# Kernel optimization log

Hardware: AMD Instinct MI355X
Metric: run time of the kernel (lower is better)

The kernel has to match this reference:

```python
import jax, jax.numpy as jnp
import numpy as np

B, N, D, H = 4, 4096, 512, 8
K = D // H  # per-head dim = 64


def setup_inputs() -> dict:
    key = jax.random.key(0)
    k1, k2, k3, k4 = jax.random.split(key, 4)
    x = jax.random.normal(k1, (B, N, D), dtype=jnp.float32)
    # Conv1d(D, K, 1, bias=False) -> weight matrix [K, D], kaiming fan_out
    Wa = jax.random.normal(k2, (K, D), dtype=jnp.float32) * np.float32(np.sqrt(2.0 / K))
    # Conv1d(K, 1, 1) -> weight vector [K], bias scalar (init 0.01)
    Wb = jax.random.normal(k3, (K,), dtype=jnp.float32) * np.float32(np.sqrt(2.0))
    Wc = jax.random.normal(k4, (K,), dtype=jnp.float32) * np.float32(np.sqrt(2.0))
    wb_bias = jnp.full((), 0.01, dtype=jnp.float32)
    wc_bias = jnp.full((), 0.01, dtype=jnp.float32)
    bias = jnp.full((K,), 0.01, dtype=jnp.float32)
    return {"batchinput": x, "Wa": Wa, "Wb": Wb, "wb_bias": wb_bias,
            "Wc": Wc, "wc_bias": wc_bias, "bias": bias}


def reference(batchinput, Wa, Wb, wb_bias, Wc, wc_bias, bias):
    # single step (n_steps=1); all n_head heads share weights, so mean over
    # identical heads equals one head (dropout=0.0 -> identity).
    h = jnp.einsum('bnd,kd->bnk', batchinput, Wa)            # [B,N,K] projected feats
    t1 = jnp.einsum('bnk,k->bn', h, Wb) + wb_bias            # [B,N]
    t2 = jnp.einsum('bnk,k->bn', h, Wc) + wc_bias            # [B,N]
    scores = t1[:, :, None] + t2[:, None, :]                 # [B,N,N] additive score
    coefs = jax.nn.softmax(jax.nn.leaky_relu(scores, negative_slope=0.2), axis=-1)
    out = jnp.einsum('bnm,bmk->bnk', coefs, h) + bias        # [B,N,K]
    return out
```

## Files before the change

kernel.cpp:

```cpp
#include <hip/hip_runtime.h>
#include <hip/hip_bf16.h>

constexpr int cB = 4;
constexpr int cN = 4096;
constexpr int cD = 512;
constexpr int cK = 64;
constexpr int cNB = cB * cN;
constexpr int cNP = cN + 1;
constexpr int cCS = 16;
constexpr int cNC = cN / cCS;
constexpr int cNC1 = cNC + 1;

typedef unsigned short u16;
typedef unsigned int u32;
typedef unsigned long long u64;
typedef __bf16 bf16x8 __attribute__((ext_vector_type(8)));
typedef float f32x4 __attribute__((ext_vector_type(4)));

constexpr size_t OFF_H    = 0;
constexpr size_t OFF_T1   = OFF_H    + (size_t)cNB * cK;
constexpr size_t OFF_T2   = OFF_T1   + cNB;
constexpr size_t OFF_T2S  = OFF_T2   + cNB;
constexpr size_t OFF_IDX  = OFF_T2S  + cNB;
constexpr size_t OFF_P    = OFF_IDX  + cNB;
constexpr size_t OFF_EPL  = OFF_P    + cNB;
constexpr size_t OFF_GNL  = OFF_EPL  + (size_t)cB * cNP * cK;
constexpr size_t OFF_EPS  = OFF_GNL  + (size_t)cB * cNP * cK;
constexpr size_t OFF_GNS  = OFF_EPS  + (size_t)cB * cNP;
constexpr size_t OFF_CHE  = OFF_GNS  + (size_t)cB * cNP;
constexpr size_t OFF_CHG  = OFF_CHE  + (size_t)cB * cNC * cK;
constexpr size_t OFF_CHES = OFF_CHG  + (size_t)cB * cNC * cK;
constexpr size_t OFF_CHGS = OFF_CHES + (size_t)cB * cNC;
constexpr size_t OFF_OFE  = OFF_CHGS + (size_t)cB * cNC;
constexpr size_t OFF_OFG  = OFF_OFE  + (size_t)cB * cNC1 * cK;
constexpr size_t OFF_OFES = OFF_OFG  + (size_t)cB * cNC1 * cK;
constexpr size_t OFF_OFGS = OFF_OFES + (size_t)cB * cNC1;
constexpr size_t OFF_WB16 = OFF_OFGS + (size_t)cB * cNC1;

__device__ __forceinline__ u16 f2bf(float f) {
    unsigned u = __float_as_uint(f);
    u += 0x7fffu + ((u >> 16) & 1u);
    return (u16)(u >> 16);
}
__device__ __forceinline__ u32 pk2(float a, float b) {
    return (u32)f2bf(a) | ((u32)f2bf(b) << 16);
}
__device__ __forceinline__ u32 f2sort(float f) {
    u32 b = __float_as_uint(f);
    u32 mask = (u32)((int)b >> 31);
    return b ^ (mask | 0x80000000u);
}

__global__ __launch_bounds__(256) void k_prep(
    const float* __restrict__ x, const float* __restrict__ Wa,
    const float* __restrict__ Wb, const float* __restrict__ wbb,
    const float* __restrict__ Wc, const float* __restrict__ wcb,
    u16* __restrict__ wab16, float* __restrict__ t1, float* __restrict__ t2)
{
    __shared__ float wabL[cD], wacL[cD];
    int t = threadIdx.x;
    if (blockIdx.x >= 512) {
        int i4 = (((int)blockIdx.x - 512) * 256 + t) * 4;
        float4 v = *(const float4*)(Wa + i4);
        uint2 p = {pk2(v.x, v.y), pk2(v.z, v.w)};
        *(uint2*)(wab16 + i4) = p;
        return;
    }
    float s1a = 0.f, s2a = 0.f, s1b = 0.f, s2b = 0.f;
#pragma unroll 8
    for (int k = 0; k < cK; ++k) {
        float wbk = Wb[k], wck = Wc[k];
        float wa1 = Wa[k * cD + t];
        float wa2 = Wa[k * cD + t + 256];
        s1a += wa1 * wbk; s2a += wa1 * wck;
        s1b += wa2 * wbk; s2b += wa2 * wck;
    }
    wabL[t] = s1a; wacL[t] = s2a; wabL[t + 256] = s1b; wacL[t + 256] = s2b;
    __syncthreads();

    int w = t >> 6, lane = t & 63;
    int d1 = lane * 4, d2 = 256 + lane * 4;
    float4 wbA = *(const float4*)&wabL[d1], wbB = *(const float4*)&wabL[d2];
    float4 wcA = *(const float4*)&wacL[d1], wcB = *(const float4*)&wacL[d2];
    float wbbv = wbb[0], wcbv = wcb[0];
#pragma unroll 2
    for (int rr = 0; rr < 8; ++rr) {
        int row = blockIdx.x * 32 + w * 8 + rr;
        const float* xp = x + (size_t)row * cD;
        float4 a  = *(const float4*)(xp + d1);
        float4 bq = *(const float4*)(xp + d2);
        float p1 = a.x*wbA.x + a.y*wbA.y + a.z*wbA.z + a.w*wbA.w
                 + bq.x*wbB.x + bq.y*wbB.y + bq.z*wbB.z + bq.w*wbB.w;
        float p2 = a.x*wcA.x + a.y*wcA.y + a.z*wcA.z + a.w*wcA.w
                 + bq.x*wcB.x + bq.y*wcB.y + bq.z*wcB.z + bq.w*wcB.w;
#pragma unroll
        for (int off = 32; off > 0; off >>= 1) {
            p1 += __shfl_down(p1, off, 64);
            p2 += __shfl_down(p2, off, 64);
        }
        if (lane == 0) { t1[row] = p1 + wbbv; t2[row] = p2 + wcbv; }
    }
}

__global__ __launch_bounds__(256) void k_projrank(
    const float* __restrict__ x, const u16* __restrict__ wab16,
    const float* __restrict__ t1, const float* __restrict__ t2,
    float* __restrict__ h, float* __restrict__ t2s, int* __restrict__ idxs,
    int* __restrict__ pidx)
{
    __shared__ __align__(16) u64 shbuf[4096 + 256];
    int t = threadIdx.x;
    if (blockIdx.x < 256) {
        int rowbase = blockIdx.x * 64;
        int w = t >> 6, lane = t & 63, m = lane & 15, quad = lane >> 4;
        const float* xg = x + (size_t)(rowbase + w * 16 + m) * cD + quad * 8;
        const u16* wg = wab16 + (size_t)m * cD + quad * 8;

        f32x4 acc[4] = {{0.f,0.f,0.f,0.f},{0.f,0.f,0.f,0.f},
                        {0.f,0.f,0.f,0.f},{0.f,0.f,0.f,0.f}};
#pragma unroll 4
        for (int s = 0; s < 16; ++s) {
            float4 xa  = *(const float4*)(xg + s * 32);
            float4 xb2 = *(const float4*)(xg + s * 32 + 4);
            uint4 xv = {pk2(xa.x, xa.y), pk2(xa.z, xa.w),
                        pk2(xb2.x, xb2.y), pk2(xb2.z, xb2.w)};
            bf16x8 av;
            __builtin_memcpy(&av, &xv, 16);
#pragma unroll
            for (int g = 0; g < 4; ++g) {
                uint4 wv = *(const uint4*)(wg + (size_t)g * 16 * cD + s * 32);
                bf16x8 bv;
                __builtin_memcpy(&bv, &wv, 16);
                acc[g] = __builtin_amdgcn_mfma_f32_16x16x32_bf16(av, bv, acc[g], 0, 0, 0);
            }
        }
#pragma unroll
        for (int g = 0; g < 4; ++g) {
#pragma unroll
            for (int r4 = 0; r4 < 4; ++r4) {
                int row = w * 16 + quad * 4 + r4;
                h[(size_t)(rowbase + row) * cK + g * 16 + m] = acc[g][r4];
            }
        }
    } else {
        u64* keys = shbuf;
        int* part = (int*)(shbuf + 4096);
        int rb = blockIdx.x - 256;
        int b = rb >> 6;
        int rowgrp = rb & 63;
        for (int i = t; i < cN; i += 256)
            keys[i] = ((u64)f2sort(t2[b * cN + i]) << 32) | (u32)i;
        __syncthreads();
        int lane = t & 63, subset = t >> 6;
        int myrow = rowgrp * 64 + lane;
        u64 mykey = keys[myrow];
        u32 pk_hi = f2sort(-t1[(size_t)b * cN + myrow]);
        int s0 = subset * 1024;
        int cnt = 0, cnt2 = 0;
#pragma unroll 8
        for (int kk = 0; kk < 1024; ++kk) {
            u64 kv = keys[s0 + kk];
            cnt  += (kv < mykey) ? 1 : 0;
            cnt2 += ((u32)(kv >> 32) < pk_hi) ? 1 : 0;
        }
        part[subset * 64 + lane] = cnt;
        part[256 + subset * 64 + lane] = cnt2;
        __syncthreads();
        if (t < 64) {
            int jj = rowgrp * 64 + t;
            int rank = part[t] + part[64 + t] + part[128 + t] + part[192 + t];
            int pc   = part[256 + t] + part[320 + t] + part[384 + t] + part[448 + t];
            t2s[b * cN + rank] = t2[b * cN + jj];
            idxs[b * cN + rank] = jj;
            pidx[b * cN + jj] = pc;
        }
    }
}

__global__ __launch_bounds__(128) void k_chunkscan(
    const float* __restrict__ t2s, const int* __restrict__ idxs,
    const float* __restrict__ h,
    float* __restrict__ EpL, float* __restrict__ GnL,
    float* __restrict__ eps_l, float* __restrict__ gns_l,
    float* __restrict__ chE, float* __restrict__ chG,
    float* __restrict__ chEs, float* __restrict__ chGs)
{
    __shared__ float hs[cCS][cK];
    int t = threadIdx.x;
    int lane = t & 63, w = t >> 6;
    int unit = blockIdx.x;
    int c = unit & (cNC - 1);
    int b = unit >> 8;
    int base = b * cN + c * cCS;
    size_t rowbase = ((size_t)b * cNP + c * cCS) * cK;
    int sbase = b * cNP + c * cCS;
    float M2 = t2s[b * cN + cN - 1];
    int   idxv = (lane < 8) ? idxs[base + w * 8 + lane] : 0;
    float t2v  = (lane < cCS) ? t2s[base + lane] : 0.f;

#pragma unroll
    for (int ii = 0; ii < 8; ++ii) {
        int j = __shfl(idxv, ii, 64);
        hs[w * 8 + ii][lane] = h[((size_t)b * cN + j) * cK + lane];
    }
    float slope = w ? 0.2f : 1.0f;
    float ev[cCS];
#pragma unroll
    for (int i = 0; i < cCS; ++i)
        ev[i] = __expf(slope * (__shfl(t2v, i, 64) - M2));
    __syncthreads();

    if (w == 0) {
        if (c == cNC - 1) {
            EpL[((size_t)b * cNP + cN) * cK + lane] = 0.f;
            if (lane == 0) eps_l[b * cNP + cN] = 0.f;
        }
        float acc = 0.f, accs = 0.f;
#pragma unroll
        for (int i = cCS - 1; i >= 0; --i) {
            acc += ev[i] * hs[i][lane]; accs += ev[i];
            EpL[rowbase + (size_t)i * cK + lane] = acc;
            if (lane == 0) eps_l[sbase + i] = accs;
        }
        chE[((size_t)b * cNC + c) * cK + lane] = acc;
        if (lane == 0) chEs[b * cNC + c] = accs;
    } else {
        if (c == cNC - 1) {
            GnL[((size_t)b * cNP + cN) * cK + lane] = 0.f;
            if (lane == 0) gns_l[b * cNP + cN] = 0.f;
        }
        float acc = 0.f, accs = 0.f;
#pragma unroll
        for (int i = 0; i < cCS; ++i) {
            GnL[rowbase + (size_t)i * cK + lane] = acc;
            if (lane == 0) gns_l[sbase + i] = accs;
            acc += ev[i] * hs[i][lane]; accs += ev[i];
        }
        chG[((size_t)b * cNC + c) * cK + lane] = acc;
        if (lane == 0) chGs[b * cNC + c] = accs;
    }
}

constexpr unsigned SMEM_OUT = 134664;
__global__ __launch_bounds__(256, 1) void k_outf(
    const float* __restrict__ t1, const float* __restrict__ t2s,
    const int* __restrict__ pidx,
    const float* __restrict__ EpL, const float* __restrict__ GnL,
    const float* __restrict__ eps_l, const float* __restrict__ gns_l,
    const float* __restrict__ chE, const float* __restrict__ chG,
    const float* __restrict__ chEs, const float* __restrict__ chGs,
    const float* __restrict__ bias, float* __restrict__ out)
{
    extern __shared__ char sm[];
    float (*ofEl)[64] = (float(*)[64])(sm);
    float (*ofGl)[64] = (float(*)[64])(sm + 65792);
    float* ofEsL      = (float*)(sm + 131584);
    float* ofGsL      = (float*)(sm + 132612);
    float (*wsum)[64] = (float(*)[64])(sm + 133640);

    int t = threadIdx.x, lane = t & 63, w = t >> 6;
    int blk = blockIdx.x;
    int b = blk >> 6;
    const float* chEb = chE + (size_t)b * cNC * cK;
    const float* chGb = chG + (size_t)b * cNC * cK;
    int c0 = w * 64;

    {
        float cv[64]; float s = 0.f;
#pragma unroll
        for (int i = 0; i < 64; ++i) { cv[i] = chEb[(size_t)(c0 + i) * cK + lane]; s += cv[i]; }
        wsum[w][lane] = s;
        if (w == 0) {
            float e0 = chEs[b*cNC + lane*4+0], e1 = chEs[b*cNC + lane*4+1];
            float e2 = chEs[b*cNC + lane*4+2], e3 = chEs[b*cNC + lane*4+3];
            float p = e0+e1+e2+e3, s2 = p;
#pragma unroll
            for (int off = 1; off < 64; off <<= 1) {
                float tv = __shfl_down(s2, off, 64);
                if (lane + off < 64) s2 += tv;
            }
            float excl = s2 - p;
            ofEsL[lane*4+0] = excl + e1 + e2 + e3;
            ofEsL[lane*4+1] = excl + e2 + e3;
            ofEsL[lane*4+2] = excl + e3;
            ofEsL[lane*4+3] = excl;
            if (lane == 0) ofEsL[cNC] = 0.f;
        } else if (w == 1) {
            float e0 = chGs[b*cNC + lane*4+0], e1 = chGs[b*cNC + lane*4+1];
            float e2 = chGs[b*cNC + lane*4+2], e3 = chGs[b*cNC + lane*4+3];
            float p = e0+e1+e2+e3, s2 = p;
#pragma unroll
            for (int off = 1; off < 64; off <<= 1) {
                float tv = __shfl_up(s2, off, 64);
                if (lane >= off) s2 += tv;
            }
            float excl = s2 - p;
            ofGsL[lane*4+0] = excl;
            ofGsL[lane*4+1] = excl + e0;
            ofGsL[lane*4+2] = excl + e0 + e1;
            ofGsL[lane*4+3] = excl + e0 + e1 + e2;
            if (lane == 63) ofGsL[cNC] = s2;
        }
        __syncthreads();
        float base = 0.f;
        for (int w2 = w + 1; w2 < 4; ++w2) base += wsum[w2][lane];
        float run = base;
#pragma unroll
        for (int i = 63; i >= 0; --i) { ofEl[c0 + i][lane] = run; run += cv[i]; }
        if (w == 0) ofEl[cNC][lane] = 0.f;
    }
    __syncthreads();
    {
        float cv[64]; float s = 0.f;
#pragma unroll
        for (int i = 0; i < 64; ++i) { cv[i] = chGb[(size_t)(c0 + i) * cK + lane]; s += cv[i]; }
        wsum[w][lane] = s;
        __syncthreads();
        float base = 0.f;
        for (int w2 = 0; w2 < w; ++w2) base += wsum[w2][lane];
        float run = base;
#pragma unroll
        for (int i = 0; i < 64; ++i) { ofGl[c0 + i][lane] = run; run += cv[i]; }
        if (w == 3) ofGl[cNC][lane] = run;
    }
    __syncthreads();

    float bv = bias[lane];
    float M2 = t2s[(size_t)b * cN + cN - 1];
    int r0 = blk * 64 + w * 16;
    const float* epsb = eps_l + (size_t)b * cNP;
    const float* gnsb = gns_l + (size_t)b * cNP;
#pragma unroll 8
    for (int i = 0; i < 16; ++i) {
        int r = r0 + i;
        float T1 = t1[r];
        float smax = T1 + M2;
        float m = fmaxf(smax, 0.2f * smax);
        float A  = __expf(smax - m);
        float Cc = __expf(0.2f * smax - m);
        int p = pidx[r];
        int c = p >> 4;
        size_t pr = ((size_t)b * cNP + p) * cK + lane;
        float num = A * (EpL[pr] + ofEl[c][lane]) + Cc * (GnL[pr] + ofGl[c][lane]);
        float den = A * (epsb[p] + ofEsL[c]) + Cc * (gnsb[p] + ofGsL[c]);
        out[(size_t)r * cK + lane] = num / den + bv;
    }
}

__global__ __launch_bounds__(1024) void k_offsets(
    const float* __restrict__ chE, const float* __restrict__ chG,
    const float* __restrict__ chEs, const float* __restrict__ chGs,
    float* __restrict__ ofE, float* __restrict__ ofG,
    float* __restrict__ ofEs, float* __restrict__ ofGs)
{
    __shared__ float wsum[16][64];
    int t = threadIdx.x;
    int lane = t & 63, w = t >> 6;
    int dir = blockIdx.x & 1;
    int b = blockIdx.x >> 1;
    const float* ch = dir ? chG : chE;
    float* of = dir ? ofG : ofE;
    int c0 = w * 16;

    float cv[16];
    float s = 0.f;
#pragma unroll
    for (int i = 0; i < 16; ++i) {
        cv[i] = ch[((size_t)b * cNC + c0 + i) * cK + lane];
        s += cv[i];
    }
    wsum[w][lane] = s;
    __syncthreads();
    float base = 0.f;
    if (dir == 0) { for (int w2 = w + 1; w2 < 16; ++w2) base += wsum[w2][lane]; }
    else          { for (int w2 = 0; w2 < w; ++w2) base += wsum[w2][lane]; }

    if (dir == 0) {
        float run = base;
#pragma unroll
        for (int i = 15; i >= 0; --i) {
            of[((size_t)b * cNC1 + c0 + i) * cK + lane] = run;
            run += cv[i];
        }
        if (w == 0) of[((size_t)b * cNC1 + cNC) * cK + lane] = 0.f;
    } else {
        float run = base;
#pragma unroll
        for (int i = 0; i < 16; ++i) {
            of[((size_t)b * cNC1 + c0 + i) * cK + lane] = run;
            run += cv[i];
        }
        if (w == 15) of[((size_t)b * cNC1 + cNC) * cK + lane] = run;
    }

    if (w == 0) {
        const float* chs = dir ? chGs : chEs;
        float* ofs = dir ? ofGs : ofEs;
        float e0 = chs[b * cNC + lane * 4 + 0];
        float e1 = chs[b * cNC + lane * 4 + 1];
        float e2 = chs[b * cNC + lane * 4 + 2];
        float e3 = chs[b * cNC + lane * 4 + 3];
        float p = e0 + e1 + e2 + e3;
        if (dir == 0) {
            float s2 = p;
#pragma unroll
            for (int off = 1; off < 64; off <<= 1) {
                float tv = __shfl_down(s2, off, 64);
                if (lane + off < 64) s2 += tv;
            }
            float excl = s2 - p;
            ofs[b * cNC1 + lane * 4 + 0] = excl + e1 + e2 + e3;
            ofs[b * cNC1 + lane * 4 + 1] = excl + e2 + e3;
            ofs[b * cNC1 + lane * 4 + 2] = excl + e3;
            ofs[b * cNC1 + lane * 4 + 3] = excl;
            if (lane == 0) ofs[b * cNC1 + cNC] = 0.f;
        } else {
            float s2 = p;
#pragma unroll
            for (int off = 1; off < 64; off <<= 1) {
                float tv = __shfl_up(s2, off, 64);
                if (lane >= off) s2 += tv;
            }
            float excl = s2 - p;
            ofs[b * cNC1 + lane * 4 + 0] = excl;
            ofs[b * cNC1 + lane * 4 + 1] = excl + e0;
            ofs[b * cNC1 + lane * 4 + 2] = excl + e0 + e1;
            ofs[b * cNC1 + lane * 4 + 3] = excl + e0 + e1 + e2;
            if (lane == 63) ofs[b * cNC1 + cNC] = s2;
        }
    }
}

__global__ __launch_bounds__(256) void k_out(
    const float* __restrict__ t1, const float* __restrict__ t2s,
    const int* __restrict__ pidx,
    const float* __restrict__ EpL, const float* __restrict__ GnL,
    const float* __restrict__ eps_l, const float* __restrict__ gns_l,
    const float* __restrict__ ofE, const float* __restrict__ ofG,
    const float* __restrict__ ofEs, const float* __restrict__ ofGs,
    const float* __restrict__ bias, float* __restrict__ out)
{
    int tid = threadIdx.x;
    int lane = tid & 63;
    int r = blockIdx.x * 4 + (tid >> 6);
    int b = r >> 12;
    float T1 = t1[r];
    float M2 = t2s[b * cN + cN - 1];
    float smax = T1 + M2;
    float m = fmaxf(smax, 0.2f * smax);
    float A  = __expf(smax - m);
    float Cc = __expf(0.2f * smax - m);
    int p = pidx[r];
    int c = p >> 4;
    size_t pr = ((size_t)b * cNP + p) * cK + lane;
    size_t cr = ((size_t)b * cNC1 + c) * cK + lane;
    float num = A * (EpL[pr] + ofE[cr]) + Cc * (GnL[pr] + ofG[cr]);
    float den = A * (eps_l[(size_t)b * cNP + p] + ofEs[b * cNC1 + c])
              + Cc * (gns_l[(size_t)b * cNP + p] + ofGs[b * cNC1 + c]);
    out[(size_t)r * cK + lane] = num / den + bias[lane];
}

extern "C" void kernel_launch(void* const* d_in, const int* in_sizes, int n_in,
                              void* d_out, int out_size, void* d_ws, size_t ws_size,
                              hipStream_t stream)
{
    const float* x    = (const float*)d_in[0];
    const float* Wa   = (const float*)d_in[1];
    const float* Wb   = (const float*)d_in[2];
    const float* wbb  = (const float*)d_in[3];
    const float* Wc   = (const float*)d_in[4];
    const float* wcb  = (const float*)d_in[5];
    const float* bias = (const float*)d_in[6];
    float* out = (float*)d_out;

    float* ws = (float*)d_ws;
    float* h     = ws + OFF_H;
    float* t1    = ws + OFF_T1;
    float* t2    = ws + OFF_T2;
    float* t2s   = ws + OFF_T2S;
    int*   idxs  = (int*)(ws + OFF_IDX);
    int*   pidx  = (int*)(ws + OFF_P);
    float* EpL   = ws + OFF_EPL;
    float* GnL   = ws + OFF_GNL;
    float* eps_l = ws + OFF_EPS;
    float* gns_l = ws + OFF_GNS;
    float* chE   = ws + OFF_CHE;
    float* chG   = ws + OFF_CHG;
    float* chEs  = ws + OFF_CHES;
    float* chGs  = ws + OFF_CHGS;
    float* ofE   = ws + OFF_OFE;
    float* ofG   = ws + OFF_OFG;
    float* ofEs  = ws + OFF_OFES;
    float* ofGs  = ws + OFF_OFGS;
    u16*   wab16 = (u16*)(ws + OFF_WB16);

    static int use_big_lds = -1;
    if (use_big_lds < 0) {
        hipError_t e = hipFuncSetAttribute((const void*)k_outf,
            hipFuncAttributeMaxDynamicSharedMemorySize, (int)SMEM_OUT);
        use_big_lds = (e == hipSuccess) ? 1 : 0;
    }

    k_prep<<<544, 256, 0, stream>>>(x, Wa, Wb, wbb, Wc, wcb, wab16, t1, t2);
    k_projrank<<<512, 256, 0, stream>>>(x, wab16, t1, t2, h, t2s, idxs, pidx);
    k_chunkscan<<<cB * cNC, 128, 0, stream>>>(t2s, idxs, h, EpL, GnL, eps_l, gns_l,
                                              chE, chG, chEs, chGs);
    if (use_big_lds) {
        k_outf<<<256, 256, SMEM_OUT, stream>>>(t1, t2s, pidx, EpL, GnL, eps_l, gns_l,
                                               chE, chG, chEs, chGs, bias, out);
    } else {
        k_offsets<<<cB * 2, 1024, 0, stream>>>(chE, chG, chEs, chGs, ofE, ofG, ofEs, ofGs);
        k_out<<<cNB / 4, 256, 0, stream>>>(t1, t2s, pidx, EpL, GnL, eps_l, gns_l,
                                           ofE, ofG, ofEs, ofGs, bias, out);
    }
}
```

Before: 126.8 us.

## Move projection GEMM into prep kernel and shrink rank keys to 32-bit

The MFMA projection that computes h moves into the first kernel and converts Wa to bf16 on the fly, which drops the separate bf16 weight buffer and its conversion blocks. The rank kernel now handles only ranking, using 32-bit keys in shared memory with an index tie-break and vectorized uint4 reads instead of packed 64-bit keys. The aim is to cut LDS traffic and comparison cost in the ranking loop and to rebalance work across launches. In exchange, every projection block repeats the Wa fp32-to-bf16 conversion and reads fp32 weights, which doubles the weight traffic.

```diff
diff --git a/kernel.cpp b/kernel.cpp
--- a/kernel.cpp
+++ b/kernel.cpp
@@ -35,7 +35,6 @@
 constexpr size_t OFF_OFG  = OFF_OFE  + (size_t)cB * cNC1 * cK;
 constexpr size_t OFF_OFES = OFF_OFG  + (size_t)cB * cNC1 * cK;
 constexpr size_t OFF_OFGS = OFF_OFES + (size_t)cB * cNC1;
-constexpr size_t OFF_WB16 = OFF_OFGS + (size_t)cB * cNC1;
 
 __device__ __forceinline__ u16 f2bf(float f) {
     unsigned u = __float_as_uint(f);
@@ -51,19 +50,49 @@
     return b ^ (mask | 0x80000000u);
 }
 
-__global__ __launch_bounds__(256) void k_prep(
+__global__ __launch_bounds__(256) void k_prepg(
     const float* __restrict__ x, const float* __restrict__ Wa,
     const float* __restrict__ Wb, const float* __restrict__ wbb,
     const float* __restrict__ Wc, const float* __restrict__ wcb,
-    u16* __restrict__ wab16, float* __restrict__ t1, float* __restrict__ t2)
+    float* __restrict__ t1, float* __restrict__ t2, float* __restrict__ h)
 {
     __shared__ float wabL[cD], wacL[cD];
     int t = threadIdx.x;
     if (blockIdx.x >= 512) {
-        int i4 = (((int)blockIdx.x - 512) * 256 + t) * 4;
-        float4 v = *(const float4*)(Wa + i4);
-        uint2 p = {pk2(v.x, v.y), pk2(v.z, v.w)};
-        *(uint2*)(wab16 + i4) = p;
+        int rowbase = ((int)blockIdx.x - 512) * 64;
+        int w = t >> 6, lane = t & 63, m = lane & 15, quad = lane >> 4;
+        const float* xg = x + (size_t)(rowbase + w * 16 + m) * cD + quad * 8;
+        const float* wg = Wa + (size_t)m * cD + quad * 8;
+
+        f32x4 acc[4] = {{0.f,0.f,0.f,0.f},{0.f,0.f,0.f,0.f},
+                        {0.f,0.f,0.f,0.f},{0.f,0.f,0.f,0.f}};
+#pragma unroll 4
+        for (int s = 0; s < 16; ++s) {
+            float4 xa  = *(const float4*)(xg + s * 32);
+            float4 xb2 = *(const float4*)(xg + s * 32 + 4);
+            uint4 xv = {pk2(xa.x, xa.y), pk2(xa.z, xa.w),
+                        pk2(xb2.x, xb2.y), pk2(xb2.z, xb2.w)};
+            bf16x8 av;
+            __builtin_memcpy(&av, &xv, 16);
+#pragma unroll
+            for (int g = 0; g < 4; ++g) {
+                float4 wa1 = *(const float4*)(wg + (size_t)g * 16 * cD + s * 32);
+                float4 wa2 = *(const float4*)(wg + (size_t)g * 16 * cD + s * 32 + 4);
+                uint4 wv = {pk2(wa1.x, wa1.y), pk2(wa1.z, wa1.w),
+                            pk2(wa2.x, wa2.y), pk2(wa2.z, wa2.w)};
+                bf16x8 bv;
+                __builtin_memcpy(&bv, &wv, 16);
+                acc[g] = __builtin_amdgcn_mfma_f32_16x16x32_bf16(av, bv, acc[g], 0, 0, 0);
+            }
+        }
+#pragma unroll
+        for (int g = 0; g < 4; ++g) {
+#pragma unroll
+            for (int r4 = 0; r4 < 4; ++r4) {
+                int row = w * 16 + quad * 4 + r4;
+                h[(size_t)(rowbase + row) * cK + g * 16 + m] = acc[g][r4];
+            }
+        }
         return;
     }
     float s1a = 0.f, s2a = 0.f, s1b = 0.f, s2b = 0.f;
@@ -102,78 +131,48 @@
     }
 }
 
-__global__ __launch_bounds__(256) void k_projrank(
-    const float* __restrict__ x, const u16* __restrict__ wab16,
+__global__ __launch_bounds__(256) void k_rank(
     const float* __restrict__ t1, const float* __restrict__ t2,
-    float* __restrict__ h, float* __restrict__ t2s, int* __restrict__ idxs,
-    int* __restrict__ pidx)
-{
-    __shared__ __align__(16) u64 shbuf[4096 + 256];
+    float* __restrict__ t2s, int* __restrict__ idxs, int* __restrict__ pidx)
+{
+    __shared__ __align__(16) u32 his[cN];
+    __shared__ int part[512];
     int t = threadIdx.x;
-    if (blockIdx.x < 256) {
-        int rowbase = blockIdx.x * 64;
-        int w = t >> 6, lane = t & 63, m = lane & 15, quad = lane >> 4;
-        const float* xg = x + (size_t)(rowbase + w * 16 + m) * cD + quad * 8;
-        const u16* wg = wab16 + (size_t)m * cD + quad * 8;
-
-        f32x4 acc[4] = {{0.f,0.f,0.f,0.f},{0.f,0.f,0.f,0.f},
-                        {0.f,0.f,0.f,0.f},{0.f,0.f,0.f,0.f}};
+    int b = (int)blockIdx.x >> 6;
+    int rowgrp = (int)blockIdx.x & 63;
+    const float* t2b = t2 + (size_t)b * cN;
+    for (int i = t; i < cN; i += 256)
+        his[i] = f2sort(t2b[i]);
+    __syncthreads();
+    int lane = t & 63, subset = t >> 6;
+    int myrow = rowgrp * 64 + lane;
+    u32 myhi = his[myrow];
+    u32 pk_hi = f2sort(-t1[(size_t)b * cN + myrow]);
+    int s0 = subset * 1024;
+    int cnt = 0, cnt2 = 0;
 #pragma unroll 4
-        for (int s = 0; s < 16; ++s) {
-            float4 xa  = *(const float4*)(xg + s * 32);
-            float4 xb2 = *(const float4*)(xg + s * 32 + 4);
-            uint4 xv = {pk2(xa.x, xa.y), pk2(xa.z, xa.w),
-                        pk2(xb2.x, xb2.y), pk2(xb2.z, xb2.w)};
-            bf16x8 av;
-            __builtin_memcpy(&av, &xv, 16);
-#pragma unroll
-            for (int g = 0; g < 4; ++g) {
-                uint4 wv = *(const uint4*)(wg + (size_t)g * 16 * cD + s * 32);
-                bf16x8 bv;
-                __builtin_memcpy(&bv, &wv, 16);
-                acc[g] = __builtin_amdgcn_mfma_f32_16x16x32_bf16(av, bv, acc[g], 0, 0, 0);
-            }
-        }
-#pragma unroll
-        for (int g = 0; g < 4; ++g) {
-#pragma unroll
-            for (int r4 = 0; r4 < 4; ++r4) {
-                int row = w * 16 + quad * 4 + r4;
-                h[(size_t)(rowbase + row) * cK + g * 16 + m] = acc[g][r4];
-            }
-        }
-    } else {
-        u64* keys = shbuf;
-        int* part = (int*)(shbuf + 4096);
-        int rb = blockIdx.x - 256;
-        int b = rb >> 6;
-        int rowgrp = rb & 63;
-        for (int i = t; i < cN; i += 256)
-            keys[i] = ((u64)f2sort(t2[b * cN + i]) << 32) | (u32)i;
-        __syncthreads();
-        int lane = t & 63, subset = t >> 6;
-        int myrow = rowgrp * 64 + lane;
-        u64 mykey = keys[myrow];
-        u32 pk_hi = f2sort(-t1[(size_t)b * cN + myrow]);
-        int s0 = subset * 1024;
-        int cnt = 0, cnt2 = 0;
-#pragma unroll 8
-        for (int kk = 0; kk < 1024; ++kk) {
-            u64 kv = keys[s0 + kk];
-            cnt  += (kv < mykey) ? 1 : 0;
-            cnt2 += ((u32)(kv >> 32) < pk_hi) ? 1 : 0;
-        }
-        part[subset * 64 + lane] = cnt;
-        part[256 + subset * 64 + lane] = cnt2;
-        __syncthreads();
-        if (t < 64) {
-            int jj = rowgrp * 64 + t;
-            int rank = part[t] + part[64 + t] + part[128 + t] + part[192 + t];
-            int pc   = part[256 + t] + part[320 + t] + part[384 + t] + part[448 + t];
-            t2s[b * cN + rank] = t2[b * cN + jj];
-            idxs[b * cN + rank] = jj;
-            pidx[b * cN + jj] = pc;
-        }
+    for (int kk = 0; kk < 1024; kk += 4) {
+        uint4 kv = *(const uint4*)&his[s0 + kk];
+        int j0 = s0 + kk;
+        cnt  += (kv.x < myhi || (kv.x == myhi && j0 + 0 < myrow)) ? 1 : 0;
+        cnt  += (kv.y < myhi || (kv.y == myhi && j0 + 1 < myrow)) ? 1 : 0;
+        cnt  += (kv.z < myhi || (kv.z == myhi && j0 + 2 < myrow)) ? 1 : 0;
+        cnt  += (kv.w < myhi || (kv.w == myhi && j0 + 3 < myrow)) ? 1 : 0;
+        cnt2 += (kv.x < pk_hi) ? 1 : 0;
+        cnt2 += (kv.y < pk_hi) ? 1 : 0;
+        cnt2 += (kv.z < pk_hi) ? 1 : 0;
+        cnt2 += (kv.w < pk_hi) ? 1 : 0;
+    }
+    part[subset * 64 + lane] = cnt;
+    part[256 + subset * 64 + lane] = cnt2;
+    __syncthreads();
+    if (t < 64) {
+        int jj = rowgrp * 64 + t;
+        int rank = part[t] + part[64 + t] + part[128 + t] + part[192 + t];
+        int pc   = part[256 + t] + part[320 + t] + part[384 + t] + part[448 + t];
+        t2s[(size_t)b * cN + rank] = t2b[jj];
+        idxs[(size_t)b * cN + rank] = jj;
+        pidx[(size_t)b * cN + jj] = pc;
     }
 }
 
@@ -492,7 +491,6 @@
     float* ofG   = ws + OFF_OFG;
     float* ofEs  = ws + OFF_OFES;
     float* ofGs  = ws + OFF_OFGS;
-    u16*   wab16 = (u16*)(ws + OFF_WB16);
 
     static int use_big_lds = -1;
     if (use_big_lds < 0) {
@@ -501,8 +499,8 @@
         use_big_lds = (e == hipSuccess) ? 1 : 0;
     }
 
-    k_prep<<<544, 256, 0, stream>>>(x, Wa, Wb, wbb, Wc, wcb, wab16, t1, t2);
-    k_projrank<<<512, 256, 0, stream>>>(x, wab16, t1, t2, h, t2s, idxs, pidx);
+    k_prepg<<<768, 256, 0, stream>>>(x, Wa, Wb, wbb, Wc, wcb, t1, t2, h);
+    k_rank<<<256, 256, 0, stream>>>(t1, t2, t2s, idxs, pidx);
     k_chunkscan<<<cB * cNC, 128, 0, stream>>>(t2s, idxs, h, EpL, GnL, eps_l, gns_l,
                                               chE, chG, chEs, chGs);
     if (use_big_lds) {
```

After: 149.8 us. 1.18x slower.
